# Kernel tuning notes

Measured on AMD Instinct MI355X. Metric: run time of the kernel, lower is better.

Reference implementation:

```python
import jax, jax.numpy as jnp
import numpy as np


def setup_inputs() -> dict:
    key = jax.random.key(0)
    # qkv: [B, 3*C, T] with B=32 (batch*heads), C=64 head channels, T=2048 tokens
    qkv = jax.random.normal(key, (32, 192, 2048), dtype=jnp.float32)
    return {"qkv": qkv}


def reference(qkv):
    channel = qkv.shape[1] // 3
    q, k, v = jnp.split(qkv, 3, axis=1)  # each [B, C, T]
    scale = 1.0 / np.sqrt(np.sqrt(channel))  # applied to both q and k (total 1/sqrt(C))
    # scores: [B, T, S]
    attn_score = jnp.einsum('bct,bcs->bts', q * scale, k * scale)
    attn_score = jax.nn.softmax(attn_score.astype(jnp.float32), axis=-1).astype(attn_score.dtype)
    # output: [B, C, T]
    return jnp.einsum('bts,bcs->bct', attn_score, v)
```

## Files before the change

### kernel.cpp

```cpp
#include <hip/hip_runtime.h>

#define B_ 32
#define C_ 64
#define T_ 2048
#define TM 128
#define TN 64
#define NT (T_ / TN)

typedef __bf16 bf16x8 __attribute__((ext_vector_type(8)));
typedef float f32x4 __attribute__((ext_vector_type(4)));

__device__ __forceinline__ unsigned cvtpk(float lo, float hi) {
  unsigned r;
  asm("v_cvt_pk_bf16_f32 %0, %1, %2" : "=v"(r) : "v"(lo), "v"(hi));
  return r;
}
__device__ __forceinline__ float exp2v(float x) {
  float r;
  asm("v_exp_f32 %0, %1" : "=v"(r) : "v"(x));
  return r;
}


__global__ __launch_bounds__(128, 1) void attn4(const float* __restrict__ qkv,
                                                float* __restrict__ out) {
  __shared__ __align__(16) char smem[2][2][64 * 128];

  const int tid = threadIdx.x;
  const int nb = (blockIdx.x & 7) * 64 + (blockIdx.x >> 3);
  const int b = nb >> 4;
  const int t0 = (nb & 15) * TM;

  const float* qb = qkv + (size_t)b * (3 * C_ * T_);
  const float* kb = qb + C_ * T_;
  const float* vb = qb + 2 * C_ * T_;
  const float qscale = 0.18033688011112042f;

  const int l = tid & 63;
  const int w = tid >> 6;
  const int lr = l & 15;
  const int lh = l >> 4;
  const int t0w = t0 + w * 64;

  const int offA = lr * 128 + (((lh ^ (lr & 7)) & 7) << 4);
  const int offB = lr * 128 + ((((4 + lh) ^ (lr & 7)) & 7) << 4);

  bf16x8 qf[4][2];
#pragma unroll
  for (int tq = 0; tq < 4; ++tq)
#pragma unroll
    for (int h = 0; h < 2; ++h) {
      float qv[8];
#pragma unroll
      for (int j = 0; j < 8; ++j)
        qv[j] = qb[(size_t)(h * 32 + lh * 8 + j) * T_ + t0w + tq * 16 + lr] * qscale;
      union { unsigned u[4]; bf16x8 v; } tmp;
#pragma unroll
      for (int j = 0; j < 4; ++j) tmp.u[j] = cvtpk(qv[2 * j], qv[2 * j + 1]);
      qf[tq][h] = tmp.v;
    }

  const int cb = (tid >> 4) * 8;
  const int sq4 = (tid & 15) * 4;
  const int sig = (sq4 >> 5) * 4 + ((sq4 >> 2) & 3);
  const int vh8 = ((sq4 >> 4) & 1) * 8;

  f32x4 kreg[8], vreg[8];
  auto loadK = [&](int s0) {
#pragma unroll
    for (int i = 0; i < 8; ++i)
      kreg[i] = *(const f32x4*)(kb + (size_t)(cb + i) * T_ + s0 + sq4);
  };
  auto writeK = [&](int d) {
    char* Kw = smem[d][0];
#pragma unroll
    for (int j = 0; j < 4; ++j) {
      uint4 u;
      u.x = cvtpk(kreg[0][j], kreg[1][j]);
      u.y = cvtpk(kreg[2][j], kreg[3][j]);
      u.z = cvtpk(kreg[4][j], kreg[5][j]);
      u.w = cvtpk(kreg[6][j], kreg[7][j]);
      *(uint4*)(Kw + (sq4 + j) * 128 + ((((cb >> 3) ^ ((sq4 + j) & 7)) & 7) << 4)) = u;
    }
  };
  auto loadV = [&](int s0) {
#pragma unroll
    for (int i = 0; i < 8; ++i)
      vreg[i] = *(const f32x4*)(vb + (size_t)(cb + i) * T_ + s0 + sq4);
  };
  auto writeV = [&](int d) {
    char* Vw = smem[d][1];
#pragma unroll
    for (int i = 0; i < 8; ++i) {
      const int c = cb + i;
      uint2 u;
      u.x = cvtpk(vreg[i][0], vreg[i][1]);
      u.y = cvtpk(vreg[i][2], vreg[i][3]);
      *(uint2*)(Vw + c * 128 + (((sig ^ (c & 7)) & 7) << 4) + vh8) = u;
    }
  };

  f32x4 o[4][4];
#pragma unroll
  for (int cf = 0; cf < 4; ++cf)
#pragma unroll
    for (int tq = 0; tq < 4; ++tq) o[cf][tq] = (f32x4){0.f, 0.f, 0.f, 0.f};
  float psum[4] = {0.f, 0.f, 0.f, 0.f};

  loadK(0);
  writeK(0);
  loadV(0);
  writeV(0);
  __syncthreads();

  for (int it = 0; it < NT; ++it) {
    const int d = it & 1;
    const bool pf = (it + 1 < NT);
    const int s1 = (it + 1) * TN;
    const char* Kb = smem[d][0];
    const char* Vb = smem[d][1];

    if (pf) loadK(s1);

    f32x4 sc[4][4];
#pragma unroll
    for (int ns = 0; ns < 4; ++ns) {
      const bf16x8 k0 = *(const bf16x8*)(Kb + offA + ns * 2048);
      const bf16x8 k1 = *(const bf16x8*)(Kb + offB + ns * 2048);
#pragma unroll
      for (int tq = 0; tq < 4; ++tq)
        sc[tq][ns] = __builtin_amdgcn_mfma_f32_16x16x32_bf16(
            k0, qf[tq][0], (f32x4){0.f, 0.f, 0.f, 0.f}, 0, 0, 0);
#pragma unroll
      for (int tq = 0; tq < 4; ++tq)
        sc[tq][ns] = __builtin_amdgcn_mfma_f32_16x16x32_bf16(k1, qf[tq][1], sc[tq][ns], 0, 0, 0);
    }

    if (pf) { writeK(d ^ 1); loadV(s1); }

    unsigned pd[4][2][4];
#pragma unroll
    for (int tq = 0; tq < 4; ++tq) {
      float s0 = 0.f, s1s = 0.f;
#pragma unroll
      for (int ns = 0; ns < 4; ++ns) {
        f32x4 pv;
#pragma unroll
        for (int r = 0; r < 4; ++r) pv[r] = exp2v(sc[tq][ns][r]);
        pd[tq][ns >> 1][(ns & 1) * 2 + 0] = cvtpk(pv[0], pv[1]);
        pd[tq][ns >> 1][(ns & 1) * 2 + 1] = cvtpk(pv[2], pv[3]);
        if (ns & 1) s1s += (pv[0] + pv[1]) + (pv[2] + pv[3]);
        else        s0  += (pv[0] + pv[1]) + (pv[2] + pv[3]);
      }
      psum[tq] += s0 + s1s;
    }

    if (pf) writeV(d ^ 1);

#pragma unroll
    for (int cf = 0; cf < 4; ++cf) {
      const bf16x8 vA = *(const bf16x8*)(Vb + offA + cf * 2048);
      const bf16x8 vB = *(const bf16x8*)(Vb + offB + cf * 2048);
#pragma unroll
      for (int tq = 0; tq < 4; ++tq) {
        union { unsigned u[4]; bf16x8 v; } pf0;
#pragma unroll
        for (int j = 0; j < 4; ++j) pf0.u[j] = pd[tq][0][j];
        o[cf][tq] = __builtin_amdgcn_mfma_f32_16x16x32_bf16(vA, pf0.v, o[cf][tq], 0, 0, 0);
      }
#pragma unroll
      for (int tq = 0; tq < 4; ++tq) {
        union { unsigned u[4]; bf16x8 v; } pf1;
#pragma unroll
        for (int j = 0; j < 4; ++j) pf1.u[j] = pd[tq][1][j];
        o[cf][tq] = __builtin_amdgcn_mfma_f32_16x16x32_bf16(vB, pf1.v, o[cf][tq], 0, 0, 0);
      }
    }
    __syncthreads();
  }

  float inv[4];
#pragma unroll
  for (int tq = 0; tq < 4; ++tq) {
    float s = psum[tq];
    s += __shfl_xor(s, 16, 64);
    s += __shfl_xor(s, 32, 64);
    inv[tq] = 1.0f / s;
  }
  float* ob = out + (size_t)b * (C_ * T_);
#pragma unroll
  for (int cf = 0; cf < 4; ++cf)
#pragma unroll
    for (int tq = 0; tq < 4; ++tq)
#pragma unroll
      for (int r = 0; r < 4; ++r)
        ob[(size_t)(cf * 16 + lh * 4 + r) * T_ + t0w + tq * 16 + lr] = o[cf][tq][r] * inv[tq];
}

extern "C" void kernel_launch(void* const* d_in, const int* in_sizes, int n_in,
                              void* d_out, int out_size, void* d_ws, size_t ws_size,
                              hipStream_t stream) {
  const float* qkv = (const float*)d_in[0];
  float* out = (float*)d_out;
  dim3 grid((T_ / TM) * B_);
  dim3 block(128);
  hipLaunchKernelGGL(attn4, grid, block, 0, stream, qkv, out);
}
```

Measured before the change: 63.48 us.

## Split QK and PV phases into halves, interleave exp with MFMA, add setprio

Restructures the inner loop so the QK^T and PV MFMA work is done in two halves, with the exp/bf16 conversion of one half placed between MFMA groups. Shared-memory fragment loads for K and V are hoisted into register arrays, and the global V prefetch and the K/V shared writes are moved to different points in the loop. MFMA groups are wrapped in s_setprio raises so matrix work is favoured over the other wave. The aim is to overlap transcendental VALU work and memory traffic with matrix-core work across the two waves. It costs more live registers for the hoisted fragments.

```diff
diff --git a/kernel.cpp b/kernel.cpp
--- a/kernel.cpp
+++ b/kernel.cpp
@@ -22,8 +22,8 @@
 }
 
 
-__global__ __launch_bounds__(128, 1) void attn4(const float* __restrict__ qkv,
-                                                float* __restrict__ out) {
+__global__ __launch_bounds__(128, 1) void attn10(const float* __restrict__ qkv,
+                                                 float* __restrict__ out) {
   __shared__ __align__(16) char smem[2][2][64 * 128];
 
   const int tid = threadIdx.x;
@@ -122,60 +122,105 @@
 
     if (pf) loadK(s1);
 
+    bf16x8 kf0[4], kf1[4];
+#pragma unroll
+    for (int ns = 0; ns < 4; ++ns) {
+      kf0[ns] = *(const bf16x8*)(Kb + offA + ns * 2048);
+      kf1[ns] = *(const bf16x8*)(Kb + offB + ns * 2048);
+    }
+
     f32x4 sc[4][4];
-#pragma unroll
-    for (int ns = 0; ns < 4; ++ns) {
-      const bf16x8 k0 = *(const bf16x8*)(Kb + offA + ns * 2048);
-      const bf16x8 k1 = *(const bf16x8*)(Kb + offB + ns * 2048);
+    __builtin_amdgcn_s_setprio(1);
+#pragma unroll
+    for (int ns = 0; ns < 2; ++ns) {
 #pragma unroll
       for (int tq = 0; tq < 4; ++tq)
         sc[tq][ns] = __builtin_amdgcn_mfma_f32_16x16x32_bf16(
-            k0, qf[tq][0], (f32x4){0.f, 0.f, 0.f, 0.f}, 0, 0, 0);
-#pragma unroll
-      for (int tq = 0; tq < 4; ++tq)
-        sc[tq][ns] = __builtin_amdgcn_mfma_f32_16x16x32_bf16(k1, qf[tq][1], sc[tq][ns], 0, 0, 0);
-    }
-
-    if (pf) { writeK(d ^ 1); loadV(s1); }
+            kf0[ns], qf[tq][0], (f32x4){0.f, 0.f, 0.f, 0.f}, 0, 0, 0);
+#pragma unroll
+      for (int tq = 0; tq < 4; ++tq)
+        sc[tq][ns] = __builtin_amdgcn_mfma_f32_16x16x32_bf16(kf1[ns], qf[tq][1], sc[tq][ns], 0, 0, 0);
+    }
+    __builtin_amdgcn_s_setprio(0);
+
+    bf16x8 vA[4];
+#pragma unroll
+    for (int cf = 0; cf < 4; ++cf) vA[cf] = *(const bf16x8*)(Vb + offA + cf * 2048);
+    if (pf) loadV(s1);
+
+    __builtin_amdgcn_s_setprio(1);
+#pragma unroll
+    for (int ns = 2; ns < 4; ++ns) {
+#pragma unroll
+      for (int tq = 0; tq < 4; ++tq)
+        sc[tq][ns] = __builtin_amdgcn_mfma_f32_16x16x32_bf16(
+            kf0[ns], qf[tq][0], (f32x4){0.f, 0.f, 0.f, 0.f}, 0, 0, 0);
+#pragma unroll
+      for (int tq = 0; tq < 4; ++tq)
+        sc[tq][ns] = __builtin_amdgcn_mfma_f32_16x16x32_bf16(kf1[ns], qf[tq][1], sc[tq][ns], 0, 0, 0);
+    }
+    __builtin_amdgcn_s_setprio(0);
 
     unsigned pd[4][2][4];
 #pragma unroll
     for (int tq = 0; tq < 4; ++tq) {
-      float s0 = 0.f, s1s = 0.f;
-#pragma unroll
-      for (int ns = 0; ns < 4; ++ns) {
+      float a = 0.f;
+#pragma unroll
+      for (int ns = 0; ns < 2; ++ns) {
         f32x4 pv;
 #pragma unroll
         for (int r = 0; r < 4; ++r) pv[r] = exp2v(sc[tq][ns][r]);
-        pd[tq][ns >> 1][(ns & 1) * 2 + 0] = cvtpk(pv[0], pv[1]);
-        pd[tq][ns >> 1][(ns & 1) * 2 + 1] = cvtpk(pv[2], pv[3]);
-        if (ns & 1) s1s += (pv[0] + pv[1]) + (pv[2] + pv[3]);
-        else        s0  += (pv[0] + pv[1]) + (pv[2] + pv[3]);
-      }
-      psum[tq] += s0 + s1s;
-    }
-
-    if (pf) writeV(d ^ 1);
-
-#pragma unroll
-    for (int cf = 0; cf < 4; ++cf) {
-      const bf16x8 vA = *(const bf16x8*)(Vb + offA + cf * 2048);
-      const bf16x8 vB = *(const bf16x8*)(Vb + offB + cf * 2048);
+        pd[tq][0][(ns & 1) * 2 + 0] = cvtpk(pv[0], pv[1]);
+        pd[tq][0][(ns & 1) * 2 + 1] = cvtpk(pv[2], pv[3]);
+        a += (pv[0] + pv[1]) + (pv[2] + pv[3]);
+      }
+      psum[tq] += a;
+    }
+
+    __builtin_amdgcn_s_setprio(1);
+#pragma unroll
+    for (int cf = 0; cf < 4; ++cf)
 #pragma unroll
       for (int tq = 0; tq < 4; ++tq) {
-        union { unsigned u[4]; bf16x8 v; } pf0;
-#pragma unroll
-        for (int j = 0; j < 4; ++j) pf0.u[j] = pd[tq][0][j];
-        o[cf][tq] = __builtin_amdgcn_mfma_f32_16x16x32_bf16(vA, pf0.v, o[cf][tq], 0, 0, 0);
-      }
+        union { unsigned u[4]; bf16x8 v; } p0;
+#pragma unroll
+        for (int j = 0; j < 4; ++j) p0.u[j] = pd[tq][0][j];
+        o[cf][tq] = __builtin_amdgcn_mfma_f32_16x16x32_bf16(vA[cf], p0.v, o[cf][tq], 0, 0, 0);
+      }
+    __builtin_amdgcn_s_setprio(0);
+
+    bf16x8 vB[4];
+#pragma unroll
+    for (int cf = 0; cf < 4; ++cf) vB[cf] = *(const bf16x8*)(Vb + offB + cf * 2048);
+
+#pragma unroll
+    for (int tq = 0; tq < 4; ++tq) {
+      float a = 0.f;
+#pragma unroll
+      for (int ns = 2; ns < 4; ++ns) {
+        f32x4 pv;
+#pragma unroll
+        for (int r = 0; r < 4; ++r) pv[r] = exp2v(sc[tq][ns][r]);
+        pd[tq][1][(ns & 1) * 2 + 0] = cvtpk(pv[0], pv[1]);
+        pd[tq][1][(ns & 1) * 2 + 1] = cvtpk(pv[2], pv[3]);
+        a += (pv[0] + pv[1]) + (pv[2] + pv[3]);
+      }
+      psum[tq] += a;
+    }
+
+    if (pf) { writeK(d ^ 1); writeV(d ^ 1); }
+
+    __builtin_amdgcn_s_setprio(1);
+#pragma unroll
+    for (int cf = 0; cf < 4; ++cf)
 #pragma unroll
       for (int tq = 0; tq < 4; ++tq) {
-        union { unsigned u[4]; bf16x8 v; } pf1;
-#pragma unroll
-        for (int j = 0; j < 4; ++j) pf1.u[j] = pd[tq][1][j];
-        o[cf][tq] = __builtin_amdgcn_mfma_f32_16x16x32_bf16(vB, pf1.v, o[cf][tq], 0, 0, 0);
-      }
-    }
+        union { unsigned u[4]; bf16x8 v; } p1;
+#pragma unroll
+        for (int j = 0; j < 4; ++j) p1.u[j] = pd[tq][1][j];
+        o[cf][tq] = __builtin_amdgcn_mfma_f32_16x16x32_bf16(vB[cf], p1.v, o[cf][tq], 0, 0, 0);
+      }
+    __builtin_amdgcn_s_setprio(0);
     __syncthreads();
   }
 
@@ -204,5 +249,5 @@
   float* out = (float*)d_out;
   dim3 grid((T_ / TM) * B_);
   dim3 block(128);
-  hipLaunchKernelGGL(attn4, grid, block, 0, stream, qkv, out);
-}
+  hipLaunchKernelGGL(attn10, grid, block, 0, stream, qkv, out);
+}
```

New measurement: 73.68 us. +16.1%, slower.

## Pre-convert K/V to swizzled bf16 workspace and stream via global_load_lds

Applied to the files above, without the earlier changes.

Adds a prep kernel that converts K and V once to bf16 in a workspace, already swizzled into the LDS tile layout. The attention kernel then copies tiles straight into LDS with global_load_lds, with no register staging or per-tile conversion. This removes the conversion that each of the 16 query blocks per batch repeated, and halves the bytes read for K/V. The cost is an extra launch and a workspace round trip. The old path stays as a fallback when the workspace is too small.

```diff
diff --git a/kernel.cpp b/kernel.cpp
--- a/kernel.cpp
+++ b/kernel.cpp
@@ -6,6 +6,8 @@
 #define TM 128
 #define TN 64
 #define NT (T_ / TN)
+#define KWS_BYTES ((size_t)B_ * T_ * 128)
+#define WS_NEED (2 * KWS_BYTES)
 
 typedef __bf16 bf16x8 __attribute__((ext_vector_type(8)));
 typedef float f32x4 __attribute__((ext_vector_type(4)));
@@ -20,10 +22,51 @@
   asm("v_exp_f32 %0, %1" : "=v"(r) : "v"(x));
   return r;
 }
-
-
-__global__ __launch_bounds__(128, 1) void attn4(const float* __restrict__ qkv,
-                                                float* __restrict__ out) {
+__device__ __forceinline__ void gload16(const char* g, char* l) {
+  __builtin_amdgcn_global_load_lds(
+      (const __attribute__((address_space(1))) unsigned*)g,
+      (__attribute__((address_space(3))) unsigned*)l, 16, 0, 0);
+}
+
+__global__ __launch_bounds__(256) void prep(const float* __restrict__ qkv,
+                                            char* __restrict__ ws) {
+  const int gid = blockIdx.x * 256 + threadIdx.x;
+  if (gid < B_ * T_) {
+    const int b = gid >> 11, s = gid & 2047;
+    const float* kb = qkv + (size_t)b * (3 * C_ * T_) + (size_t)C_ * T_;
+    char* row = ws + (size_t)b * (T_ * 128) + s * 128;
+#pragma unroll
+    for (int oct = 0; oct < 8; ++oct) {
+      float v[8];
+#pragma unroll
+      for (int j = 0; j < 8; ++j) v[j] = kb[(size_t)(oct * 8 + j) * T_ + s];
+      uint4 u;
+      u.x = cvtpk(v[0], v[1]); u.y = cvtpk(v[2], v[3]);
+      u.z = cvtpk(v[4], v[5]); u.w = cvtpk(v[6], v[7]);
+      *(uint4*)(row + (((oct ^ (s & 7)) & 7) << 4)) = u;
+    }
+  } else {
+    const int g2 = gid - B_ * T_;
+    const int b = g2 >> 11, rem = g2 & 2047, k0 = rem >> 6, c = rem & 63;
+    const float* vp = qkv + (size_t)b * (3 * C_ * T_) + 2 * (size_t)C_ * T_ +
+                      (size_t)c * T_ + k0 * 64;
+    char* row = ws + KWS_BYTES + (size_t)b * (T_ * 128) + k0 * 8192 + c * 128;
+#pragma unroll
+    for (int g = 0; g < 16; ++g) {
+      const int sl = g * 4;
+      const f32x4 v = *(const f32x4*)(vp + sl);
+      uint2 u;
+      u.x = cvtpk(v[0], v[1]); u.y = cvtpk(v[2], v[3]);
+      const int sig = (sl >> 5) * 4 + ((sl >> 2) & 3);
+      *(uint2*)(row + (((sig ^ (c & 7)) & 7) << 4) + ((sl >> 4) & 1) * 8) = u;
+    }
+  }
+}
+
+__global__ __launch_bounds__(128, 1) void attn11(const float* __restrict__ qkv,
+                                                 const char* __restrict__ kws,
+                                                 const char* __restrict__ vws,
+                                                 float* __restrict__ out) {
   __shared__ __align__(16) char smem[2][2][64 * 128];
 
   const int tid = threadIdx.x;
@@ -32,8 +75,6 @@
   const int t0 = (nb & 15) * TM;
 
   const float* qb = qkv + (size_t)b * (3 * C_ * T_);
-  const float* kb = qb + C_ * T_;
-  const float* vb = qb + 2 * C_ * T_;
   const float qscale = 0.18033688011112042f;
 
   const int l = tid & 63;
@@ -60,11 +101,147 @@
       qf[tq][h] = tmp.v;
     }
 
+  const char* kgb = kws + (size_t)b * (T_ * 128);
+  const char* vgb = vws + (size_t)b * (T_ * 128);
+  auto stage = [&](int s0, int d) {
+    const char* kg = kgb + s0 * 128 + w * 4096 + l * 16;
+    const char* vg = vgb + (s0 >> 6) * 8192 + w * 4096 + l * 16;
+    char* kl = &smem[d][0][w * 4096];
+    char* vl = &smem[d][1][w * 4096];
+#pragma unroll
+    for (int ch = 0; ch < 4; ++ch) {
+      gload16(kg + ch * 1024, kl + ch * 1024);
+      gload16(vg + ch * 1024, vl + ch * 1024);
+    }
+  };
+
+  f32x4 o[4][4];
+#pragma unroll
+  for (int cf = 0; cf < 4; ++cf)
+#pragma unroll
+    for (int tq = 0; tq < 4; ++tq) o[cf][tq] = (f32x4){0.f, 0.f, 0.f, 0.f};
+  float psum[4] = {0.f, 0.f, 0.f, 0.f};
+
+  stage(0, 0);
+  asm volatile("s_waitcnt vmcnt(0)" ::: "memory");
+  __syncthreads();
+
+  for (int it = 0; it < NT; ++it) {
+    const int d = it & 1;
+    const bool pf = (it + 1 < NT);
+    const char* Kb = smem[d][0];
+    const char* Vb = smem[d][1];
+
+    if (pf) stage((it + 1) * TN, d ^ 1);
+
+    f32x4 sc[4][4];
+#pragma unroll
+    for (int ns = 0; ns < 4; ++ns) {
+      const bf16x8 k0 = *(const bf16x8*)(Kb + offA + ns * 2048);
+      const bf16x8 k1 = *(const bf16x8*)(Kb + offB + ns * 2048);
+#pragma unroll
+      for (int tq = 0; tq < 4; ++tq)
+        sc[tq][ns] = __builtin_amdgcn_mfma_f32_16x16x32_bf16(
+            k0, qf[tq][0], (f32x4){0.f, 0.f, 0.f, 0.f}, 0, 0, 0);
+#pragma unroll
+      for (int tq = 0; tq < 4; ++tq)
+        sc[tq][ns] = __builtin_amdgcn_mfma_f32_16x16x32_bf16(k1, qf[tq][1], sc[tq][ns], 0, 0, 0);
+    }
+
+    unsigned pd[4][2][4];
+#pragma unroll
+    for (int tq = 0; tq < 4; ++tq) {
+      float a0 = 0.f, a1 = 0.f;
+#pragma unroll
+      for (int ns = 0; ns < 4; ++ns) {
+        f32x4 pv;
+#pragma unroll
+        for (int r = 0; r < 4; ++r) pv[r] = exp2v(sc[tq][ns][r]);
+        pd[tq][ns >> 1][(ns & 1) * 2 + 0] = cvtpk(pv[0], pv[1]);
+        pd[tq][ns >> 1][(ns & 1) * 2 + 1] = cvtpk(pv[2], pv[3]);
+        if (ns & 1) a1 += (pv[0] + pv[1]) + (pv[2] + pv[3]);
+        else        a0 += (pv[0] + pv[1]) + (pv[2] + pv[3]);
+      }
+      psum[tq] += a0 + a1;
+    }
+
+#pragma unroll
+    for (int cf = 0; cf < 4; ++cf) {
+      const bf16x8 vA = *(const bf16x8*)(Vb + offA + cf * 2048);
+      const bf16x8 vB = *(const bf16x8*)(Vb + offB + cf * 2048);
+#pragma unroll
+      for (int tq = 0; tq < 4; ++tq) {
+        union { unsigned u[4]; bf16x8 v; } p0;
+#pragma unroll
+        for (int j = 0; j < 4; ++j) p0.u[j] = pd[tq][0][j];
+        o[cf][tq] = __builtin_amdgcn_mfma_f32_16x16x32_bf16(vA, p0.v, o[cf][tq], 0, 0, 0);
+      }
+#pragma unroll
+      for (int tq = 0; tq < 4; ++tq) {
+        union { unsigned u[4]; bf16x8 v; } p1;
+#pragma unroll
+        for (int j = 0; j < 4; ++j) p1.u[j] = pd[tq][1][j];
+        o[cf][tq] = __builtin_amdgcn_mfma_f32_16x16x32_bf16(vB, p1.v, o[cf][tq], 0, 0, 0);
+      }
+    }
+    asm volatile("s_waitcnt vmcnt(0)" ::: "memory");
+    __syncthreads();
+  }
+
+  float inv[4];
+#pragma unroll
+  for (int tq = 0; tq < 4; ++tq) {
+    float s = psum[tq];
+    s += __shfl_xor(s, 16, 64);
+    s += __shfl_xor(s, 32, 64);
+    inv[tq] = 1.0f / s;
+  }
+  float* ob = out + (size_t)b * (C_ * T_);
+#pragma unroll
+  for (int cf = 0; cf < 4; ++cf)
+#pragma unroll
+    for (int tq = 0; tq < 4; ++tq)
+#pragma unroll
+      for (int r = 0; r < 4; ++r)
+        ob[(size_t)(cf * 16 + lh * 4 + r) * T_ + t0w + tq * 16 + lr] = o[cf][tq][r] * inv[tq];
+}
+
+__global__ __launch_bounds__(128, 1) void attn_fb(const float* __restrict__ qkv,
+                                                  float* __restrict__ out) {
+  __shared__ __align__(16) char smem[2][2][64 * 128];
+  const int tid = threadIdx.x;
+  const int nb = (blockIdx.x & 7) * 64 + (blockIdx.x >> 3);
+  const int b = nb >> 4;
+  const int t0 = (nb & 15) * TM;
+  const float* qb = qkv + (size_t)b * (3 * C_ * T_);
+  const float* kb = qb + C_ * T_;
+  const float* vb = qb + 2 * C_ * T_;
+  const float qscale = 0.18033688011112042f;
+  const int l = tid & 63;
+  const int w = tid >> 6;
+  const int lr = l & 15;
+  const int lh = l >> 4;
+  const int t0w = t0 + w * 64;
+  const int offA = lr * 128 + (((lh ^ (lr & 7)) & 7) << 4);
+  const int offB = lr * 128 + ((((4 + lh) ^ (lr & 7)) & 7) << 4);
+  bf16x8 qf[4][2];
+#pragma unroll
+  for (int tq = 0; tq < 4; ++tq)
+#pragma unroll
+    for (int h = 0; h < 2; ++h) {
+      float qv[8];
+#pragma unroll
+      for (int j = 0; j < 8; ++j)
+        qv[j] = qb[(size_t)(h * 32 + lh * 8 + j) * T_ + t0w + tq * 16 + lr] * qscale;
+      union { unsigned u[4]; bf16x8 v; } tmp;
+#pragma unroll
+      for (int j = 0; j < 4; ++j) tmp.u[j] = cvtpk(qv[2 * j], qv[2 * j + 1]);
+      qf[tq][h] = tmp.v;
+    }
   const int cb = (tid >> 4) * 8;
   const int sq4 = (tid & 15) * 4;
   const int sig = (sq4 >> 5) * 4 + ((sq4 >> 2) & 3);
   const int vh8 = ((sq4 >> 4) & 1) * 8;
-
   f32x4 kreg[8], vreg[8];
   auto loadK = [&](int s0) {
 #pragma unroll
@@ -99,29 +276,21 @@
       *(uint2*)(Vw + c * 128 + (((sig ^ (c & 7)) & 7) << 4) + vh8) = u;
     }
   };
-
   f32x4 o[4][4];
 #pragma unroll
   for (int cf = 0; cf < 4; ++cf)
 #pragma unroll
     for (int tq = 0; tq < 4; ++tq) o[cf][tq] = (f32x4){0.f, 0.f, 0.f, 0.f};
   float psum[4] = {0.f, 0.f, 0.f, 0.f};
-
-  loadK(0);
-  writeK(0);
-  loadV(0);
-  writeV(0);
+  loadK(0); writeK(0); loadV(0); writeV(0);
   __syncthreads();
-
   for (int it = 0; it < NT; ++it) {
     const int d = it & 1;
     const bool pf = (it + 1 < NT);
     const int s1 = (it + 1) * TN;
     const char* Kb = smem[d][0];
     const char* Vb = smem[d][1];
-
     if (pf) loadK(s1);
-
     f32x4 sc[4][4];
 #pragma unroll
     for (int ns = 0; ns < 4; ++ns) {
@@ -135,13 +304,11 @@
       for (int tq = 0; tq < 4; ++tq)
         sc[tq][ns] = __builtin_amdgcn_mfma_f32_16x16x32_bf16(k1, qf[tq][1], sc[tq][ns], 0, 0, 0);
     }
-
     if (pf) { writeK(d ^ 1); loadV(s1); }
-
     unsigned pd[4][2][4];
 #pragma unroll
     for (int tq = 0; tq < 4; ++tq) {
-      float s0 = 0.f, s1s = 0.f;
+      float a0 = 0.f, a1 = 0.f;
 #pragma unroll
       for (int ns = 0; ns < 4; ++ns) {
         f32x4 pv;
@@ -149,36 +316,33 @@
         for (int r = 0; r < 4; ++r) pv[r] = exp2v(sc[tq][ns][r]);
         pd[tq][ns >> 1][(ns & 1) * 2 + 0] = cvtpk(pv[0], pv[1]);
         pd[tq][ns >> 1][(ns & 1) * 2 + 1] = cvtpk(pv[2], pv[3]);
-        if (ns & 1) s1s += (pv[0] + pv[1]) + (pv[2] + pv[3]);
-        else        s0  += (pv[0] + pv[1]) + (pv[2] + pv[3]);
-      }
-      psum[tq] += s0 + s1s;
-    }
-
+        if (ns & 1) a1 += (pv[0] + pv[1]) + (pv[2] + pv[3]);
+        else        a0 += (pv[0] + pv[1]) + (pv[2] + pv[3]);
+      }
+      psum[tq] += a0 + a1;
+    }
     if (pf) writeV(d ^ 1);
-
 #pragma unroll
     for (int cf = 0; cf < 4; ++cf) {
       const bf16x8 vA = *(const bf16x8*)(Vb + offA + cf * 2048);
       const bf16x8 vB = *(const bf16x8*)(Vb + offB + cf * 2048);
 #pragma unroll
       for (int tq = 0; tq < 4; ++tq) {
-        union { unsigned u[4]; bf16x8 v; } pf0;
-#pragma unroll
-        for (int j = 0; j < 4; ++j) pf0.u[j] = pd[tq][0][j];
-        o[cf][tq] = __builtin_amdgcn_mfma_f32_16x16x32_bf16(vA, pf0.v, o[cf][tq], 0, 0, 0);
+        union { unsigned u[4]; bf16x8 v; } p0;
+#pragma unroll
+        for (int j = 0; j < 4; ++j) p0.u[j] = pd[tq][0][j];
+        o[cf][tq] = __builtin_amdgcn_mfma_f32_16x16x32_bf16(vA, p0.v, o[cf][tq], 0, 0, 0);
       }
 #pragma unroll
       for (int tq = 0; tq < 4; ++tq) {
-        union { unsigned u[4]; bf16x8 v; } pf1;
-#pragma unroll
-        for (int j = 0; j < 4; ++j) pf1.u[j] = pd[tq][1][j];
-        o[cf][tq] = __builtin_amdgcn_mfma_f32_16x16x32_bf16(vB, pf1.v, o[cf][tq], 0, 0, 0);
+        union { unsigned u[4]; bf16x8 v; } p1;
+#pragma unroll
+        for (int j = 0; j < 4; ++j) p1.u[j] = pd[tq][1][j];
+        o[cf][tq] = __builtin_amdgcn_mfma_f32_16x16x32_bf16(vB, p1.v, o[cf][tq], 0, 0, 0);
       }
     }
     __syncthreads();
   }
-
   float inv[4];
 #pragma unroll
   for (int tq = 0; tq < 4; ++tq) {
@@ -202,7 +366,12 @@
                               hipStream_t stream) {
   const float* qkv = (const float*)d_in[0];
   float* out = (float*)d_out;
-  dim3 grid((T_ / TM) * B_);
-  dim3 block(128);
-  hipLaunchKernelGGL(attn4, grid, block, 0, stream, qkv, out);
-}
+  if (ws_size >= WS_NEED) {
+    char* ws = (char*)d_ws;
+    hipLaunchKernelGGL(prep, dim3(2 * B_ * T_ / 256), dim3(256), 0, stream, qkv, ws);
+    hipLaunchKernelGGL(attn11, dim3((T_ / TM) * B_), dim3(128), 0, stream, qkv,
+                       (const char*)ws, (const char*)(ws + KWS_BYTES), out);
+  } else {
+    hipLaunchKernelGGL(attn_fb, dim3((T_ / TM) * B_), dim3(128), 0, stream, qkv, out);
+  }
+}
```

Measured after the change: 88.38 us. +39.2%, slower.
